# Performance work log

Hardware: AMD Instinct MI355X
Metric: run time of the kernel (lower is better)

The kernel has to match this reference:

```python
import jax, jax.numpy as jnp
import numpy as np

N, L, V = 8192, 50, 50000   # sentences, max words/sentence, vocab
D, H, O = 300, 150, 64      # embed dim, SAGE hidden, SAGE out
THRESH = 0.7
NEG = -1e9


def _sage_pool(h, A, mask, W1s, W1n, b1, W2s, W2n, b2, gw, gb):
    """Two-layer mean-aggregator SAGEConv + GlobalAttentionPooling, vectorized
    over N independent per-sentence graphs.
    h:[N,L,din] node feats, A:[N,L,L] bool adjacency (src u -> dst v), mask:[N,L] valid nodes."""
    Af = A.astype(h.dtype)
    deg = jnp.maximum(Af.sum(axis=1), 1.0)  # in-degree per dst node [N,L]

    def conv(x, Ws, Wn, b):
        m = jnp.einsum('nuv,nud->nvd', Af, x) / deg[..., None]  # mean of in-neighbors
        return x @ Ws + m @ Wn + b  # fc_self(x) + fc_neigh(mean)

    h1 = jax.nn.relu(conv(h, W1s, W1n, b1))
    h2 = conv(h1, W2s, W2n, b2)
    # global attention pooling: softmax(gate) over real nodes of each graph
    gate = jnp.squeeze(h2 @ gw, -1) + gb  # [N,L]
    attn = jax.nn.softmax(jnp.where(mask, gate, NEG), axis=-1)
    return jnp.einsum('nl,nld->nd', attn, h2)  # [N,O]


def setup_inputs() -> dict:
    key = jax.random.key(0)
    ks = jax.random.split(key, 32)
    pos = jnp.arange(L)
    lengths = jax.random.randint(ks[0], (N,), 5, L + 1)
    valid = pos[None, :] < lengths[:, None]  # [N,L] real-word mask (0 = pad)
    words = jax.random.randint(ks[1], (N, L), 1, V) * valid
    syntax_words = jax.random.randint(ks[2], (N, L), 1, V) * valid
    adj = jax.random.uniform(ks[3], (N, L, L)) < 0.08
    syntax_adj = (adj & valid[:, :, None] & valid[:, None, :]).astype(jnp.int32)
    hsg_feature = jax.random.normal(ks[4], (N, O), jnp.float32)

    def lin(k, i, o):
        return jax.random.normal(k, (i, o), jnp.float32) / np.sqrt(i)

    inp = {
        'words': words.astype(jnp.int32),
        'syntax_words': syntax_words.astype(jnp.int32),
        'syntax_adj': syntax_adj,
        'hsg_feature': hsg_feature,
        'embed': jax.random.normal(ks[5], (V, D), jnp.float32) * 0.1,
        'sem_W1s': lin(ks[6], D, H), 'sem_W1n': lin(ks[7], D, H), 'sem_b1': jnp.zeros((H,), jnp.float32),
        'sem_W2s': lin(ks[8], H, O), 'sem_W2n': lin(ks[9], H, O), 'sem_b2': jnp.zeros((O,), jnp.float32),
        'sem_gw': lin(ks[10], O, 1), 'sem_gb': jnp.zeros((1,), jnp.float32),
        'syn_W1s': lin(ks[11], D, H), 'syn_W1n': lin(ks[12], D, H), 'syn_b1': jnp.zeros((H,), jnp.float32),
        'syn_W2s': lin(ks[13], H, O), 'syn_W2n': lin(ks[14], H, O), 'syn_b2': jnp.zeros((O,), jnp.float32),
        'syn_gw': lin(ks[15], O, 1), 'syn_gb': jnp.zeros((1,), jnp.float32),
        'cls_w1': lin(ks[16], 3 * O, 128), 'cls_b1': jnp.zeros((128,), jnp.float32),
        'cls_w2': lin(ks[17], 128, 2), 'cls_b2': jnp.zeros((2,), jnp.float32),
    }
    return inp


def reference(words, syntax_words, syntax_adj, hsg_feature, embed,
              sem_W1s, sem_W1n, sem_b1, sem_W2s, sem_W2n, sem_b2, sem_gw, sem_gb,
              syn_W1s, syn_W1n, syn_b1, syn_W2s, syn_W2n, syn_b2, syn_gw, syn_gb,
              cls_w1, cls_b1, cls_w2, cls_b2):
    # --- semantic graph: per-sentence cosine-similarity thresholding ---
    mask = words > 0
    emb = embed[words]  # [N,L,D] gather
    nrm = emb / jnp.maximum(jnp.linalg.norm(emb, axis=-1, keepdims=True), 1e-8)
    cos = jnp.einsum('nld,nmd->nlm', nrm, nrm)  # [N,L,L]
    semA = (cos > THRESH) & mask[:, :, None] & mask[:, None, :]  # includes self-loops (cos=1)
    sem_feat = _sage_pool(emb, semA, mask,
                          sem_W1s, sem_W1n, sem_b1, sem_W2s, sem_W2n, sem_b2, sem_gw, sem_gb)
    # --- syntax graph: given per-sentence adjacency over its word ids ---
    syn_mask = syntax_words > 0
    syn_emb = embed[syntax_words]
    syn_feat = _sage_pool(syn_emb, syntax_adj.astype(bool), syn_mask,
                          syn_W1s, syn_W1n, syn_b1, syn_W2s, syn_W2n, syn_b2, syn_gw, syn_gb)
    # --- concat with HSG sentence state, classify ---
    feat = jnp.concatenate([sem_feat, syn_feat, hsg_feature], axis=-1)  # [N,192]
    hid = jax.nn.relu(feat @ cls_w1 + cls_b1)
    return hid @ cls_w2 + cls_b2  # [N,2]
```

## Files before the change

kernel.cpp:

```cpp
#include <hip/hip_runtime.h>

#define NS 8192
#define L  50

typedef unsigned short u16;
typedef unsigned int   u32;
typedef __attribute__((ext_vector_type(8))) __bf16 bf16x8;
typedef __attribute__((ext_vector_type(4))) float  f32x4;

#define OFF_X    0
#define OFF_TT   0
#define OFF_T2T  0
#define OFF_RED  9216
#define OFF_H1   21760
#define OFF_M    43264
#define OFF_DIAG 43264
#define OFF_WID  52480
#define OFF_CLO  52736
#define OFF_CHI  52992
#define OFF_RDEG 53248
#define SMEM_SZ  53504

#define XSTR  328
#define TSTR  68
#define H1STR 168
#define MSTR  72
#define RSTR  20

#define W1_ROWS 320
#define W1_KP   328
#define W2_ROWS 128
#define W2_KP   168
#define W1SZ (W1_ROWS * W1_KP)
#define W2SZ (W2_ROWS * W2_KP)

__device__ __forceinline__ u16 f2bf(float f) {
  u32 u = __float_as_uint(f);
  u += 0x7fffu + ((u >> 16) & 1u);
  return (u16)(u >> 16);
}
__device__ __forceinline__ f32x4 mfma16(bf16x8 a, bf16x8 b, f32x4 c) {
  return __builtin_amdgcn_mfma_f32_16x16x32_bf16(a, b, c, 0, 0, 0);
}
__device__ __forceinline__ uint2 pack4bf(f32x4 c) {
  uint2 p;
  p.x = (u32)f2bf(c[0]) | ((u32)f2bf(c[1]) << 16);
  p.y = (u32)f2bf(c[2]) | ((u32)f2bf(c[3]) << 16);
  return p;
}
union BF8U { bf16x8 v; uint4 u; };
__device__ __forceinline__ bf16x8 ld_bf8_b64pair(const u16* p) {
  uint2 a = *(const uint2*)p;
  uint2 b = *(const uint2*)(p + 4);
  BF8U r; r.u = make_uint4(a.x, a.y, b.x, b.y);
  return r.v;
}

struct GParams {
  const int* words; const int* syn_words; const int* syn_adj;
  const float* embed;
  const float* sem_b1; const float* sem_b2; const float* sem_gw; const float* sem_gb;
  const float* syn_b1; const float* syn_b2; const float* syn_gw; const float* syn_gb;
  const u16* w1t_sem; const u16* w1t_syn; const u16* w2t_sem; const u16* w2t_syn;
  float* semf; float* synf;
};

#define AGG_SLOT(ACCSLOT, GT)                                                \
  {                                                                          \
    const int gg = (GT);                                                     \
    const u16* tb = tt + (gg * 16 + ln) * TSTR + quad * 8;                   \
    bf16x8 ta0 = ld_bf8_b64pair(tb);                                         \
    bf16x8 ta1 = ld_bf8_b64pair(tb + 32);                                    \
    f32x4 gacc[4] = {z4, z4, z4, z4};                                        \
    _Pragma("unroll")                                                        \
    for (int vt = 0; vt < 4; ++vt) {                                         \
      gacc[vt] = mfma16(ta0, mb0[vt], gacc[vt]);                             \
      gacc[vt] = mfma16(ta1, mb1[vt], gacc[vt]);                             \
    }                                                                        \
    const int j0 = gg * 16 + quad * 4;                                       \
    float bv[4];                                                             \
    _Pragma("unroll")                                                        \
    for (int r = 0; r < 4; ++r) { int j = j0 + r; bv[r] = (j < 150) ? b1g[j] : 0.f; } \
    _Pragma("unroll")                                                        \
    for (int vt = 0; vt < 4; ++vt) {                                         \
      const int v = vt * 16 + ln;                                            \
      f32x4 hv;                                                              \
      _Pragma("unroll")                                                      \
      for (int r = 0; r < 4; ++r)                                            \
        hv[r] = fmaxf(ACCSLOT[vt][r] + gacc[vt][r] * rd[vt] + bv[r], 0.f);   \
      *(uint2*)(h1p + v * H1STR + j0) = pack4bf(hv);                         \
    }                                                                        \
  }

__global__ __launch_bounds__(256, 3) void sage_kernel(GParams P) {
  __shared__ __align__(16) char smem[SMEM_SZ];
  int*   wid   = (int*)(smem + OFF_WID);
  u32*   clo   = (u32*)(smem + OFF_CLO);
  u32*   chi   = (u32*)(smem + OFF_CHI);
  float* rdegp = (float*)(smem + OFF_RDEG);
  float* diag  = (float*)(smem + OFF_DIAG);

  const int tid  = threadIdx.x;
  const int lane = tid & 63;
  const int w    = tid >> 6;
  const int ln   = lane & 15;
  const int quad = lane >> 4;

  const bool semg = (blockIdx.x < NS);
  const int  n    = semg ? blockIdx.x : (blockIdx.x - NS);

  const int*   wsrc = semg ? P.words   : P.syn_words;
  const u16*   W1T  = semg ? P.w1t_sem : P.w1t_syn;
  const u16*   W2T  = semg ? P.w2t_sem : P.w2t_syn;
  const float* b1g  = semg ? P.sem_b1  : P.syn_b1;
  const float* b2g  = semg ? P.sem_b2  : P.syn_b2;
  const float* gw   = semg ? P.sem_gw  : P.syn_gw;
  const float* gb   = semg ? P.sem_gb  : P.syn_gb;
  float* featout    = semg ? P.semf    : P.synf;

  {
    int wd = 0;
    {
      const int v = w + 4 * ln;
      if (lane < 16 && v < L) wd = wsrc[(size_t)n * L + v];
    }
    for (int i = 0; i < 16; ++i) {
      const int v = w + 4 * i;
      const int word = __shfl(wd, i);
      const float* src = P.embed + (size_t)word * 300;
      u16* xrow = (u16*)(smem + OFF_X) + v * XSTR;
      for (int l = lane; l < 82; l += 64) {
        uint2 pk = make_uint2(0u, 0u);
        if (word > 0 && l < 75) {
          float4 f = *(const float4*)(src + l * 4);
          u32 ax = __float_as_uint(f.x) + 0x8000u;
          u32 ay = __float_as_uint(f.y) + 0x8000u;
          u32 az = __float_as_uint(f.z) + 0x8000u;
          u32 aw = __float_as_uint(f.w) + 0x8000u;
          pk.x = (ax >> 16) | (ay & 0xffff0000u);
          pk.y = (az >> 16) | (aw & 0xffff0000u);
        }
        *(uint2*)(xrow + l * 4) = pk;
      }
    }
    if (tid < 64) {
      wid[tid] = (tid < L) ? wsrc[(size_t)n * L + tid] : 0;
      clo[tid] = 0u; chi[tid] = 0u;
    }
  }
  __syncthreads();

  const f32x4 z4 = {0.f, 0.f, 0.f, 0.f};

  if (semg) {
    f32x4 g[4] = {z4, z4, z4, z4};
    const char* xb = smem + OFF_X;
    const int arow = (w * 16 + ln) * (XSTR * 2) + quad * 16;
    for (int kk = 0; kk < 10; ++kk) {
      bf16x8 a = *(const bf16x8*)(xb + arow + kk * 64);
      #pragma unroll
      for (int nt = 0; nt < 4; ++nt) {
        bf16x8 b = *(const bf16x8*)(xb + (nt * 16 + ln) * (XSTR * 2) + quad * 16 + kk * 64);
        g[nt] = mfma16(a, b, g[nt]);
      }
    }
    {
      const int r = ln - quad * 4;
      if (r >= 0 && r < 4) {
        #pragma unroll
        for (int nt = 0; nt < 4; ++nt) {
          if (nt == w) {
            float val = (r == 0) ? g[nt][0] : (r == 1) ? g[nt][1]
                      : (r == 2) ? g[nt][2] : g[nt][3];
            diag[w * 16 + ln] = val;
          }
        }
      }
    }
    __syncthreads();
    {
      const int ubase = w * 16 + quad * 4;
      float ru[4]; int uok[4];
      #pragma unroll
      for (int r = 0; r < 4; ++r) {
        ru[r] = rsqrtf(fmaxf(diag[ubase + r], 1e-12f));
        uok[r] = wid[ubase + r] > 0;
      }
      #pragma unroll
      for (int nt = 0; nt < 4; ++nt) {
        const int v = nt * 16 + ln;
        const float rv = rsqrtf(fmaxf(diag[v], 1e-12f));
        const bool vok = wid[v] > 0;
        u32 nib = 0u;
        #pragma unroll
        for (int r = 0; r < 4; ++r) {
          float c = g[nt][r] * ru[r] * rv;
          if (vok && uok[r] && c > 0.7f) nib |= (1u << r);
        }
        if (nib) {
          if (ubase < 32) atomicOr(&clo[v], nib << ubase);
          else            atomicOr(&chi[v], nib << (ubase - 32));
        }
      }
    }
  } else {
    const int* abase = P.syn_adj + (size_t)n * (L * L);
    for (int v = w; v < L; v += 4) {
      int val = (lane < L) ? abase[lane * L + v] : 0;
      unsigned long long m = __ballot(val != 0);
      if (lane == 0) { clo[v] = (u32)m; chi[v] = (u32)(m >> 32); }
    }
    __syncthreads();
  }
  __syncthreads();

  if (tid < 64) {
    int dg = __popc(clo[tid]) + __popc(chi[tid]);
    rdegp[tid] = 1.0f / (float)(dg > 0 ? dg : 1);
  }
  {
    const int v = lane, half = w;
    const u32 src = (half < 2) ? clo[v] : chi[v];
    const int sh = (half & 1) * 16;
    u16* Mrow = (u16*)(smem + OFF_M) + v * MSTR + half * 16;
    #pragma unroll
    for (int c = 0; c < 4; ++c) {
      uint2 pk;
      u32 b0 = (src >> (sh + 4 * c + 0)) & 1u;
      u32 b1 = (src >> (sh + 4 * c + 1)) & 1u;
      u32 b2 = (src >> (sh + 4 * c + 2)) & 1u;
      u32 b3 = (src >> (sh + 4 * c + 3)) & 1u;
      pk.x = (b0 ? 0x3F80u : 0u) | (b1 ? 0x3F800000u : 0u);
      pk.y = (b2 ? 0x3F80u : 0u) | (b3 ? 0x3F800000u : 0u);
      *(uint2*)(Mrow + 4 * c) = pk;
    }
  }

  const int rs0 = (2 * w)     * 16 + ln;
  const int rs1 = (2 * w + 1) * 16 + ln;
  const int rs2 = ((w < 2) ? (8 + w) : (16 + w)) * 16 + ln;
  const int rs3 = (10 + 2 * w) * 16 + ln;
  const int rs4 = (11 + 2 * w) * 16 + ln;
  f32x4 acc[5][4];
  #pragma unroll
  for (int i = 0; i < 5; ++i)
    #pragma unroll
    for (int m = 0; m < 4; ++m) acc[i][m] = z4;
  {
    const char* xb = smem + OFF_X;
    for (int kk = 0; kk < 10; ++kk) {
      const int wo = kk * 32 + quad * 8;
      bf16x8 x[4];
      #pragma unroll
      for (int m = 0; m < 4; ++m)
        x[m] = *(const bf16x8*)(xb + (m * 16 + ln) * (XSTR * 2) + quad * 16 + kk * 64);
      bf16x8 bf0 = *(const bf16x8*)(W1T + (size_t)rs0 * W1_KP + wo);
      bf16x8 bf1 = *(const bf16x8*)(W1T + (size_t)rs1 * W1_KP + wo);
      bf16x8 bf2 = *(const bf16x8*)(W1T + (size_t)rs2 * W1_KP + wo);
      bf16x8 bf3 = *(const bf16x8*)(W1T + (size_t)rs3 * W1_KP + wo);
      bf16x8 bf4 = *(const bf16x8*)(W1T + (size_t)rs4 * W1_KP + wo);
      #pragma unroll
      for (int m = 0; m < 4; ++m) {
        acc[0][m] = mfma16(x[m], bf0, acc[0][m]);
        acc[1][m] = mfma16(x[m], bf1, acc[1][m]);
        acc[3][m] = mfma16(bf3, x[m], acc[3][m]);
        acc[4][m] = mfma16(bf4, x[m], acc[4][m]);
      }
      if (w < 2) {
        #pragma unroll
        for (int m = 0; m < 4; ++m) acc[2][m] = mfma16(x[m], bf2, acc[2][m]);
      } else {
        #pragma unroll
        for (int m = 0; m < 4; ++m) acc[2][m] = mfma16(bf2, x[m], acc[2][m]);
      }
    }
  }
  __syncthreads();

  float rd[4];
  #pragma unroll
  for (int vt = 0; vt < 4; ++vt) rd[vt] = rdegp[vt * 16 + ln];

  {
    u16* tt = (u16*)(smem + OFF_TT);
    #pragma unroll
    for (int m = 0; m < 4; ++m) {
      const int v0 = m * 16 + quad * 4;
      *(uint2*)(tt + ((2 * w)     * 16 + ln) * TSTR + v0) = pack4bf(acc[0][m]);
      *(uint2*)(tt + ((2 * w + 1) * 16 + ln) * TSTR + v0) = pack4bf(acc[1][m]);
    }
    if (w < 2) {
      #pragma unroll
      for (int m = 0; m < 4; ++m) {
        const int v0 = m * 16 + quad * 4;
        *(uint2*)(tt + ((8 + w) * 16 + ln) * TSTR + v0) = pack4bf(acc[2][m]);
      }
    }
  }
  __syncthreads();

  {
    const u16* tt = (const u16*)(smem + OFF_TT);
    const u16* Mp = (const u16*)(smem + OFF_M);
    u16* h1p = (u16*)(smem + OFF_H1);
    bf16x8 mb0[4], mb1[4];
    #pragma unroll
    for (int vt = 0; vt < 4; ++vt) {
      mb0[vt] = *(const bf16x8*)(Mp + (vt * 16 + ln) * MSTR + quad * 8);
      mb1[vt] = *(const bf16x8*)(Mp + (vt * 16 + ln) * MSTR + quad * 8 + 32);
    }
    AGG_SLOT(acc[3], 2 * w)
    AGG_SLOT(acc[4], 2 * w + 1)
    if (w >= 2) AGG_SLOT(acc[2], 6 + w)
  }
  __syncthreads();

  f32x4 h2v[4];
  {
    f32x4 s2acc[4] = {z4, z4, z4, z4};
    f32x4 t2acc[4] = {z4, z4, z4, z4};
    const u16* h1p = (const u16*)(smem + OFF_H1);
    for (int kk = 0; kk < 5; ++kk) {
      const int wo = kk * 32 + quad * 8;
      bf16x8 h[4];
      #pragma unroll
      for (int t4 = 0; t4 < 4; ++t4)
        h[t4] = *(const bf16x8*)(h1p + (t4 * 16 + ln) * H1STR + wo);
      bf16x8 a2  = *(const bf16x8*)(W2T + (size_t)(w * 16 + ln) * W2_KP + wo);
      bf16x8 b2f = *(const bf16x8*)(W2T + (size_t)((4 + w) * 16 + ln) * W2_KP + wo);
      #pragma unroll
      for (int vt = 0; vt < 4; ++vt) {
        s2acc[vt] = mfma16(a2, h[vt], s2acc[vt]);
        t2acc[vt] = mfma16(h[vt], b2f, t2acc[vt]);
      }
    }
    u16* t2t = (u16*)(smem + OFF_T2T);
    #pragma unroll
    for (int m = 0; m < 4; ++m) {
      const int v0 = m * 16 + quad * 4;
      *(uint2*)(t2t + (w * 16 + ln) * TSTR + v0) = pack4bf(t2acc[m]);
    }
    const u16* Mp = (const u16*)(smem + OFF_M);
    f32x4 g2[4] = {z4, z4, z4, z4};
    const u16* t2b = t2t + (w * 16 + ln) * TSTR + quad * 8;
    bf16x8 u0 = ld_bf8_b64pair(t2b);
    bf16x8 u1 = ld_bf8_b64pair(t2b + 32);
    #pragma unroll
    for (int vt = 0; vt < 4; ++vt) {
      bf16x8 m0 = *(const bf16x8*)(Mp + (vt * 16 + ln) * MSTR + quad * 8);
      bf16x8 m1 = *(const bf16x8*)(Mp + (vt * 16 + ln) * MSTR + quad * 8 + 32);
      g2[vt] = mfma16(u0, m0, g2[vt]);
      g2[vt] = mfma16(u1, m1, g2[vt]);
    }
    const int j0q = w * 16 + quad * 4;
    float b2v[4];
    #pragma unroll
    for (int r = 0; r < 4; ++r) b2v[r] = b2g[j0q + r];
    #pragma unroll
    for (int vt = 0; vt < 4; ++vt)
      #pragma unroll
      for (int r = 0; r < 4; ++r)
        h2v[vt][r] = s2acc[vt][r] + g2[vt][r] * rd[vt] + b2v[r];
  }
  __syncthreads();

  {
    const int j0q = w * 16 + quad * 4;
    float gwv[4];
    #pragma unroll
    for (int r = 0; r < 4; ++r) gwv[r] = gw[j0q + r];
    float* redp = (float*)(smem + OFF_RED);
    #pragma unroll
    for (int vt = 0; vt < 4; ++vt) {
      float p = h2v[vt][0] * gwv[0] + h2v[vt][1] * gwv[1]
              + h2v[vt][2] * gwv[2] + h2v[vt][3] * gwv[3];
      redp[(vt * 16 + ln) * RSTR + (w * 4 + quad)] = p;
    }
  }
  __syncthreads();

  float attnv;
  {
    const float* redp = (const float*)(smem + OFF_RED) + lane * RSTR;
    f32x4 r0 = *(const f32x4*)(redp);
    f32x4 r1 = *(const f32x4*)(redp + 4);
    f32x4 r2 = *(const f32x4*)(redp + 8);
    f32x4 r3 = *(const f32x4*)(redp + 12);
    float g = gb[0] + r0[0] + r0[1] + r0[2] + r0[3] + r1[0] + r1[1] + r1[2] + r1[3]
            + r2[0] + r2[1] + r2[2] + r2[3] + r3[0] + r3[1] + r3[2] + r3[3];
    const bool val = wid[lane] > 0;
    g = val ? g : -1e30f;
    float mx = g;
    #pragma unroll
    for (int off = 32; off; off >>= 1) mx = fmaxf(mx, __shfl_xor(mx, off));
    float e = val ? __expf(g - mx) : 0.f;
    float ssum = e;
    #pragma unroll
    for (int off = 32; off; off >>= 1) ssum += __shfl_xor(ssum, off);
    attnv = e / ssum;
  }

  {
    float av[4];
    #pragma unroll
    for (int vt = 0; vt < 4; ++vt) av[vt] = __shfl(attnv, vt * 16 + ln);
    float xr[4];
    #pragma unroll
    for (int r = 0; r < 4; ++r) {
      float x = av[0] * h2v[0][r] + av[1] * h2v[1][r]
              + av[2] * h2v[2][r] + av[3] * h2v[3][r];
      #pragma unroll
      for (int off = 1; off < 16; off <<= 1) x += __shfl_xor(x, off);
      xr[r] = x;
    }
    if (ln == 0) {
      const int j0q = w * 16 + quad * 4;
      *(float4*)(featout + (size_t)n * 64 + j0q) = make_float4(xr[0], xr[1], xr[2], xr[3]);
    }
  }
}

__global__ void prep_all(const float* sem_W1n, const float* sem_W1s,
                         const float* syn_W1n, const float* syn_W1s,
                         const float* sem_W2s, const float* sem_W2n,
                         const float* syn_W2s, const float* syn_W2n,
                         u16* w1t_sem, u16* w1t_syn, u16* w2t_sem, u16* w2t_syn) {
  int idx = blockIdx.x * 256 + threadIdx.x;
  if (idx < 2 * W1SZ) {
    const bool sem = idx < W1SZ;
    const int li = sem ? idx : idx - W1SZ;
    const float* Wn = sem ? sem_W1n : syn_W1n;
    const float* Ws = sem ? sem_W1s : syn_W1s;
    u16* dst = sem ? w1t_sem : w1t_syn;
    int nn = li / W1_KP, k = li - nn * W1_KP;
    float v = 0.f;
    if (k < 300) {
      if (nn < 150) v = Wn[k * 150 + nn];
      else if (nn >= 160 && nn < 310) v = Ws[k * 150 + (nn - 160)];
    }
    dst[li] = f2bf(v);
  } else if (idx < 2 * W1SZ + 2 * W2SZ) {
    int j = idx - 2 * W1SZ;
    const bool sem = j < W2SZ;
    const int li = sem ? j : j - W2SZ;
    const float* Ws = sem ? sem_W2s : syn_W2s;
    const float* Wn = sem ? sem_W2n : syn_W2n;
    u16* dst = sem ? w2t_sem : w2t_syn;
    int nn = li / W2_KP, k = li - nn * W2_KP;
    float v = 0.f;
    if (k < 150) v = (nn < 64) ? Ws[k * 64 + nn] : Wn[k * 64 + (nn - 64)];
    dst[li] = f2bf(v);
  }
}

__global__ __launch_bounds__(128) void cls_kernel(const float* semf, const float* synf,
                                                  const float* hsg,
                                                  const float* w1, const float* b1,
                                                  const float* w2, const float* b2,
                                                  float* out) {
  __shared__ float feat[16][192];
  __shared__ float hid[16][132];
  const int r0 = blockIdx.x * 16;
  for (int idx = threadIdx.x; idx < 16 * 192; idx += 128) {
    int r = idx / 192, c = idx % 192;
    float v;
    if (c < 64)        v = semf[(size_t)(r0 + r) * 64 + c];
    else if (c < 128)  v = synf[(size_t)(r0 + r) * 64 + (c - 64)];
    else               v = hsg [(size_t)(r0 + r) * 64 + (c - 128)];
    feat[r][c] = v;
  }
  __syncthreads();
  {
    const int j = threadIdx.x;
    float acc[16];
    float bb = b1[j];
    #pragma unroll
    for (int r = 0; r < 16; ++r) acc[r] = bb;
    for (int k = 0; k < 192; ++k) {
      float ww = w1[(size_t)k * 128 + j];
      #pragma unroll
      for (int r = 0; r < 16; ++r) acc[r] += feat[r][k] * ww;
    }
    #pragma unroll
    for (int r = 0; r < 16; ++r) hid[r][j] = fmaxf(acc[r], 0.0f);
  }
  __syncthreads();
  if (threadIdx.x < 32) {
    const int r = threadIdx.x >> 1, o = threadIdx.x & 1;
    float a = b2[o];
    for (int h = 0; h < 128; ++h) a += hid[r][h] * w2[h * 2 + o];
    out[(size_t)(r0 + r) * 2 + o] = a;
  }
}

extern "C" void kernel_launch(void* const* d_in, const int* in_sizes, int n_in,
                              void* d_out, int out_size, void* d_ws, size_t ws_size,
                              hipStream_t stream) {
  GParams P;
  P.words     = (const int*)d_in[0];
  P.syn_words = (const int*)d_in[1];
  P.syn_adj   = (const int*)d_in[2];
  const float* hsg = (const float*)d_in[3];
  P.embed   = (const float*)d_in[4];
  const float* sem_W1s = (const float*)d_in[5];
  const float* sem_W1n = (const float*)d_in[6];
  P.sem_b1  = (const float*)d_in[7];
  const float* sem_W2s = (const float*)d_in[8];
  const float* sem_W2n = (const float*)d_in[9];
  P.sem_b2  = (const float*)d_in[10];
  P.sem_gw  = (const float*)d_in[11];
  P.sem_gb  = (const float*)d_in[12];
  const float* syn_W1s = (const float*)d_in[13];
  const float* syn_W1n = (const float*)d_in[14];
  P.syn_b1  = (const float*)d_in[15];
  const float* syn_W2s = (const float*)d_in[16];
  const float* syn_W2n = (const float*)d_in[17];
  P.syn_b2  = (const float*)d_in[18];
  P.syn_gw  = (const float*)d_in[19];
  P.syn_gb  = (const float*)d_in[20];
  const float* cls_w1 = (const float*)d_in[21];
  const float* cls_b1 = (const float*)d_in[22];
  const float* cls_w2 = (const float*)d_in[23];
  const float* cls_b2 = (const float*)d_in[24];

  float* semf = (float*)d_ws;
  float* synf = semf + (size_t)NS * 64;
  u16* w1t_sem = (u16*)((char*)d_ws + (size_t)4 * 1024 * 1024);
  u16* w1t_syn = w1t_sem + W1SZ;
  u16* w2t_sem = w1t_syn + W1SZ;
  u16* w2t_syn = w2t_sem + W2SZ;
  P.semf = semf; P.synf = synf;
  P.w1t_sem = w1t_sem; P.w1t_syn = w1t_syn;
  P.w2t_sem = w2t_sem; P.w2t_syn = w2t_syn;

  const int total = 2 * W1SZ + 2 * W2SZ;
  prep_all<<<(total + 255) / 256, 256, 0, stream>>>(
      sem_W1n, sem_W1s, syn_W1n, syn_W1s,
      sem_W2s, sem_W2n, syn_W2s, syn_W2n,
      w1t_sem, w1t_syn, w2t_sem, w2t_syn);

  sage_kernel<<<2 * NS, 256, 0, stream>>>(P);
  cls_kernel<<<NS / 16, 128, 0, stream>>>(semf, synf, hsg, cls_w1, cls_b1,
                                          cls_w2, cls_b2, (float*)d_out);
}
```

Measured before the change: 768.9 us.

## Fuse cosine Gram product into layer-1 projection loop sharing X fragment loads

The semantic-graph Gram matrix is now computed inside the same k-loop as the first-layer weight projections. Both use the same bf16 X fragments loaded once from shared memory, which removes a separate pass over X and one barrier. Each wave's column tiles are rotated through a per-wave order (ct) so that tile 0 is the wave's own diagonal block. That lets the Gram computation keep only the wave's own row block against all column tiles, and the aggregation and writes are re-indexed to match. The cost is more live accumulator registers at once (g plus acc), which may add register pressure at the given occupancy bound.

```diff
diff --git a/kernel.cpp b/kernel.cpp
--- a/kernel.cpp
+++ b/kernel.cpp
@@ -83,7 +83,7 @@
     for (int r = 0; r < 4; ++r) { int j = j0 + r; bv[r] = (j < 150) ? b1g[j] : 0.f; } \
     _Pragma("unroll")                                                        \
     for (int vt = 0; vt < 4; ++vt) {                                         \
-      const int v = vt * 16 + ln;                                            \
+      const int v = ct[vt] * 16 + ln;                                        \
       f32x4 hv;                                                              \
       _Pragma("unroll")                                                      \
       for (int r = 0; r < 4; ++r)                                            \
@@ -116,7 +116,9 @@
   const float* b2g  = semg ? P.sem_b2  : P.syn_b2;
   const float* gw   = semg ? P.sem_gw  : P.syn_gw;
   const float* gb   = semg ? P.sem_gb  : P.syn_gb;
-  float* featout    = semg ? P.semf    : P.synf;
+  float* featout    = semg ? P.semf    : P.syn_adj ? P.synf : P.synf;
+
+  const int ct[4] = {w, (w + 1) & 3, (w + 2) & 3, (w + 3) & 3};
 
   {
     int wd = 0;
@@ -152,65 +154,168 @@
 
   const f32x4 z4 = {0.f, 0.f, 0.f, 0.f};
 
-  if (semg) {
-    f32x4 g[4] = {z4, z4, z4, z4};
-    const char* xb = smem + OFF_X;
-    const int arow = (w * 16 + ln) * (XSTR * 2) + quad * 16;
-    for (int kk = 0; kk < 10; ++kk) {
-      bf16x8 a = *(const bf16x8*)(xb + arow + kk * 64);
-      #pragma unroll
-      for (int nt = 0; nt < 4; ++nt) {
-        bf16x8 b = *(const bf16x8*)(xb + (nt * 16 + ln) * (XSTR * 2) + quad * 16 + kk * 64);
-        g[nt] = mfma16(a, b, g[nt]);
-      }
-    }
-    {
-      const int r = ln - quad * 4;
-      if (r >= 0 && r < 4) {
-        #pragma unroll
-        for (int nt = 0; nt < 4; ++nt) {
-          if (nt == w) {
-            float val = (r == 0) ? g[nt][0] : (r == 1) ? g[nt][1]
-                      : (r == 2) ? g[nt][2] : g[nt][3];
-            diag[w * 16 + ln] = val;
-          }
-        }
-      }
-    }
-    __syncthreads();
-    {
-      const int ubase = w * 16 + quad * 4;
-      float ru[4]; int uok[4];
-      #pragma unroll
-      for (int r = 0; r < 4; ++r) {
-        ru[r] = rsqrtf(fmaxf(diag[ubase + r], 1e-12f));
-        uok[r] = wid[ubase + r] > 0;
-      }
-      #pragma unroll
-      for (int nt = 0; nt < 4; ++nt) {
-        const int v = nt * 16 + ln;
-        const float rv = rsqrtf(fmaxf(diag[v], 1e-12f));
-        const bool vok = wid[v] > 0;
-        u32 nib = 0u;
-        #pragma unroll
-        for (int r = 0; r < 4; ++r) {
-          float c = g[nt][r] * ru[r] * rv;
-          if (vok && uok[r] && c > 0.7f) nib |= (1u << r);
-        }
-        if (nib) {
-          if (ubase < 32) atomicOr(&clo[v], nib << ubase);
-          else            atomicOr(&chi[v], nib << (ubase - 32));
-        }
-      }
-    }
-  } else {
+  if (!semg) {
     const int* abase = P.syn_adj + (size_t)n * (L * L);
     for (int v = w; v < L; v += 4) {
       int val = (lane < L) ? abase[lane * L + v] : 0;
       unsigned long long m = __ballot(val != 0);
       if (lane == 0) { clo[v] = (u32)m; chi[v] = (u32)(m >> 32); }
     }
-    __syncthreads();
+  }
+
+  const int rs0 = (2 * w)     * 16 + ln;
+  const int rs1 = (2 * w + 1) * 16 + ln;
+  const int rs2 = ((w < 2) ? (8 + w) : (16 + w)) * 16 + ln;
+  const int rs3 = (10 + 2 * w) * 16 + ln;
+  const int rs4 = (11 + 2 * w) * 16 + ln;
+  f32x4 acc[5][4];
+  f32x4 g[4] = {z4, z4, z4, z4};
+  #pragma unroll
+  for (int i = 0; i < 5; ++i)
+    #pragma unroll
+    for (int m = 0; m < 4; ++m) acc[i][m] = z4;
+  {
+    const char* xb = smem + OFF_X;
+    const int xr0 = (ct[0] * 16 + ln) * (XSTR * 2);
+    const int xr1 = (ct[1] * 16 + ln) * (XSTR * 2);
+    const int xr2 = (ct[2] * 16 + ln) * (XSTR * 2);
+    const int xr3 = (ct[3] * 16 + ln) * (XSTR * 2);
+    if (semg) {
+      for (int kk = 0; kk < 10; ++kk) {
+        const int xo = quad * 16 + kk * 64;
+        const int wo = kk * 32 + quad * 8;
+        bf16x8 x0 = *(const bf16x8*)(xb + xr0 + xo);
+        bf16x8 x1 = *(const bf16x8*)(xb + xr1 + xo);
+        bf16x8 x2 = *(const bf16x8*)(xb + xr2 + xo);
+        bf16x8 x3 = *(const bf16x8*)(xb + xr3 + xo);
+        bf16x8 bf0 = *(const bf16x8*)(W1T + (size_t)rs0 * W1_KP + wo);
+        bf16x8 bf1 = *(const bf16x8*)(W1T + (size_t)rs1 * W1_KP + wo);
+        bf16x8 bf2 = *(const bf16x8*)(W1T + (size_t)rs2 * W1_KP + wo);
+        bf16x8 bf3 = *(const bf16x8*)(W1T + (size_t)rs3 * W1_KP + wo);
+        bf16x8 bf4 = *(const bf16x8*)(W1T + (size_t)rs4 * W1_KP + wo);
+        g[0] = mfma16(x0, x0, g[0]);
+        g[1] = mfma16(x0, x1, g[1]);
+        g[2] = mfma16(x0, x2, g[2]);
+        g[3] = mfma16(x0, x3, g[3]);
+        acc[0][0] = mfma16(x0, bf0, acc[0][0]);
+        acc[0][1] = mfma16(x1, bf0, acc[0][1]);
+        acc[0][2] = mfma16(x2, bf0, acc[0][2]);
+        acc[0][3] = mfma16(x3, bf0, acc[0][3]);
+        acc[1][0] = mfma16(x0, bf1, acc[1][0]);
+        acc[1][1] = mfma16(x1, bf1, acc[1][1]);
+        acc[1][2] = mfma16(x2, bf1, acc[1][2]);
+        acc[1][3] = mfma16(x3, bf1, acc[1][3]);
+        acc[3][0] = mfma16(bf3, x0, acc[3][0]);
+        acc[3][1] = mfma16(bf3, x1, acc[3][1]);
+        acc[3][2] = mfma16(bf3, x2, acc[3][2]);
+        acc[3][3] = mfma16(bf3, x3, acc[3][3]);
+        acc[4][0] = mfma16(bf4, x0, acc[4][0]);
+        acc[4][1] = mfma16(bf4, x1, acc[4][1]);
+        acc[4][2] = mfma16(bf4, x2, acc[4][2]);
+        acc[4][3] = mfma16(bf4, x3, acc[4][3]);
+        if (w < 2) {
+          acc[2][0] = mfma16(x0, bf2, acc[2][0]);
+          acc[2][1] = mfma16(x1, bf2, acc[2][1]);
+          acc[2][2] = mfma16(x2, bf2, acc[2][2]);
+          acc[2][3] = mfma16(x3, bf2, acc[2][3]);
+        } else {
+          acc[2][0] = mfma16(bf2, x0, acc[2][0]);
+          acc[2][1] = mfma16(bf2, x1, acc[2][1]);
+          acc[2][2] = mfma16(bf2, x2, acc[2][2]);
+          acc[2][3] = mfma16(bf2, x3, acc[2][3]);
+        }
+      }
+      const int r = ln - quad * 4;
+      if (r >= 0 && r < 4) {
+        float val = (r == 0) ? g[0][0] : (r == 1) ? g[0][1]
+                  : (r == 2) ? g[0][2] : g[0][3];
+        diag[w * 16 + ln] = val;
+      }
+    } else {
+      for (int kk = 0; kk < 10; ++kk) {
+        const int xo = quad * 16 + kk * 64;
+        const int wo = kk * 32 + quad * 8;
+        bf16x8 x0 = *(const bf16x8*)(xb + xr0 + xo);
+        bf16x8 x1 = *(const bf16x8*)(xb + xr1 + xo);
+        bf16x8 x2 = *(const bf16x8*)(xb + xr2 + xo);
+        bf16x8 x3 = *(const bf16x8*)(xb + xr3 + xo);
+        bf16x8 bf0 = *(const bf16x8*)(W1T + (size_t)rs0 * W1_KP + wo);
+        bf16x8 bf1 = *(const bf16x8*)(W1T + (size_t)rs1 * W1_KP + wo);
+        bf16x8 bf2 = *(const bf16x8*)(W1T + (size_t)rs2 * W1_KP + wo);
+        bf16x8 bf3 = *(const bf16x8*)(W1T + (size_t)rs3 * W1_KP + wo);
+        bf16x8 bf4 = *(const bf16x8*)(W1T + (size_t)rs4 * W1_KP + wo);
+        acc[0][0] = mfma16(x0, bf0, acc[0][0]);
+        acc[0][1] = mfma16(x1, bf0, acc[0][1]);
+        acc[0][2] = mfma16(x2, bf0, acc[0][2]);
+        acc[0][3] = mfma16(x3, bf0, acc[0][3]);
+        acc[1][0] = mfma16(x0, bf1, acc[1][0]);
+        acc[1][1] = mfma16(x1, bf1, acc[1][1]);
+        acc[1][2] = mfma16(x2, bf1, acc[1][2]);
+        acc[1][3] = mfma16(x3, bf1, acc[1][3]);
+        acc[3][0] = mfma16(bf3, x0, acc[3][0]);
+        acc[3][1] = mfma16(bf3, x1, acc[3][1]);
+        acc[3][2] = mfma16(bf3, x2, acc[3][2]);
+        acc[3][3] = mfma16(bf3, x3, acc[3][3]);
+        acc[4][0] = mfma16(bf4, x0, acc[4][0]);
+        acc[4][1] = mfma16(bf4, x1, acc[4][1]);
+        acc[4][2] = mfma16(bf4, x2, acc[4][2]);
+        acc[4][3] = mfma16(bf4, x3, acc[4][3]);
+        if (w < 2) {
+          acc[2][0] = mfma16(x0, bf2, acc[2][0]);
+          acc[2][1] = mfma16(x1, bf2, acc[2][1]);
+          acc[2][2] = mfma16(x2, bf2, acc[2][2]);
+          acc[2][3] = mfma16(x3, bf2, acc[2][3]);
+        } else {
+          acc[2][0] = mfma16(bf2, x0, acc[2][0]);
+          acc[2][1] = mfma16(bf2, x1, acc[2][1]);
+          acc[2][2] = mfma16(bf2, x2, acc[2][2]);
+          acc[2][3] = mfma16(bf2, x3, acc[2][3]);
+        }
+      }
+    }
+  }
+  __syncthreads();
+
+  if (semg) {
+    const int ubase = w * 16 + quad * 4;
+    float ru[4]; int uok[4];
+    #pragma unroll
+    for (int r = 0; r < 4; ++r) {
+      ru[r] = rsqrtf(fmaxf(diag[ubase + r], 1e-12f));
+      uok[r] = wid[ubase + r] > 0;
+    }
+    #pragma unroll
+    for (int j = 0; j < 4; ++j) {
+      const int v = ct[j] * 16 + ln;
+      const float rv = rsqrtf(fmaxf(diag[v], 1e-12f));
+      const bool vok = wid[v] > 0;
+      u32 nib = 0u;
+      #pragma unroll
+      for (int r = 0; r < 4; ++r) {
+        float c = g[j][r] * ru[r] * rv;
+        if (vok && uok[r] && c > 0.7f) nib |= (1u << r);
+      }
+      if (nib) {
+        if (ubase < 32) atomicOr(&clo[v], nib << ubase);
+        else            atomicOr(&chi[v], nib << (ubase - 32));
+      }
+    }
+  }
+  {
+    u16* tt = (u16*)(smem + OFF_TT);
+    #pragma unroll
+    for (int j = 0; j < 4; ++j) {
+      const int v0 = ct[j] * 16 + quad * 4;
+      *(uint2*)(tt + ((2 * w)     * 16 + ln) * TSTR + v0) = pack4bf(acc[0][j]);
+      *(uint2*)(tt + ((2 * w + 1) * 16 + ln) * TSTR + v0) = pack4bf(acc[1][j]);
+    }
+    if (w < 2) {
+      #pragma unroll
+      for (int j = 0; j < 4; ++j) {
+        const int v0 = ct[j] * 16 + quad * 4;
+        *(uint2*)(tt + ((8 + w) * 16 + ln) * TSTR + v0) = pack4bf(acc[2][j]);
+      }
+    }
   }
   __syncthreads();
 
@@ -235,79 +340,20 @@
       *(uint2*)(Mrow + 4 * c) = pk;
     }
   }
-
-  const int rs0 = (2 * w)     * 16 + ln;
-  const int rs1 = (2 * w + 1) * 16 + ln;
-  const int rs2 = ((w < 2) ? (8 + w) : (16 + w)) * 16 + ln;
-  const int rs3 = (10 + 2 * w) * 16 + ln;
-  const int rs4 = (11 + 2 * w) * 16 + ln;
-  f32x4 acc[5][4];
-  #pragma unroll
-  for (int i = 0; i < 5; ++i)
-    #pragma unroll
-    for (int m = 0; m < 4; ++m) acc[i][m] = z4;
-  {
-    const char* xb = smem + OFF_X;
-    for (int kk = 0; kk < 10; ++kk) {
-      const int wo = kk * 32 + quad * 8;
-      bf16x8 x[4];
-      #pragma unroll
-      for (int m = 0; m < 4; ++m)
-        x[m] = *(const bf16x8*)(xb + (m * 16 + ln) * (XSTR * 2) + quad * 16 + kk * 64);
-      bf16x8 bf0 = *(const bf16x8*)(W1T + (size_t)rs0 * W1_KP + wo);
-      bf16x8 bf1 = *(const bf16x8*)(W1T + (size_t)rs1 * W1_KP + wo);
-      bf16x8 bf2 = *(const bf16x8*)(W1T + (size_t)rs2 * W1_KP + wo);
-      bf16x8 bf3 = *(const bf16x8*)(W1T + (size_t)rs3 * W1_KP + wo);
-      bf16x8 bf4 = *(const bf16x8*)(W1T + (size_t)rs4 * W1_KP + wo);
-      #pragma unroll
-      for (int m = 0; m < 4; ++m) {
-        acc[0][m] = mfma16(x[m], bf0, acc[0][m]);
-        acc[1][m] = mfma16(x[m], bf1, acc[1][m]);
-        acc[3][m] = mfma16(bf3, x[m], acc[3][m]);
-        acc[4][m] = mfma16(bf4, x[m], acc[4][m]);
-      }
-      if (w < 2) {
-        #pragma unroll
-        for (int m = 0; m < 4; ++m) acc[2][m] = mfma16(x[m], bf2, acc[2][m]);
-      } else {
-        #pragma unroll
-        for (int m = 0; m < 4; ++m) acc[2][m] = mfma16(bf2, x[m], acc[2][m]);
-      }
-    }
-  }
-  __syncthreads();
-
-  float rd[4];
-  #pragma unroll
-  for (int vt = 0; vt < 4; ++vt) rd[vt] = rdegp[vt * 16 + ln];
-
-  {
-    u16* tt = (u16*)(smem + OFF_TT);
-    #pragma unroll
-    for (int m = 0; m < 4; ++m) {
-      const int v0 = m * 16 + quad * 4;
-      *(uint2*)(tt + ((2 * w)     * 16 + ln) * TSTR + v0) = pack4bf(acc[0][m]);
-      *(uint2*)(tt + ((2 * w + 1) * 16 + ln) * TSTR + v0) = pack4bf(acc[1][m]);
-    }
-    if (w < 2) {
-      #pragma unroll
-      for (int m = 0; m < 4; ++m) {
-        const int v0 = m * 16 + quad * 4;
-        *(uint2*)(tt + ((8 + w) * 16 + ln) * TSTR + v0) = pack4bf(acc[2][m]);
-      }
-    }
-  }
   __syncthreads();
 
   {
     const u16* tt = (const u16*)(smem + OFF_TT);
     const u16* Mp = (const u16*)(smem + OFF_M);
     u16* h1p = (u16*)(smem + OFF_H1);
+    float rd[4];
     bf16x8 mb0[4], mb1[4];
     #pragma unroll
     for (int vt = 0; vt < 4; ++vt) {
-      mb0[vt] = *(const bf16x8*)(Mp + (vt * 16 + ln) * MSTR + quad * 8);
-      mb1[vt] = *(const bf16x8*)(Mp + (vt * 16 + ln) * MSTR + quad * 8 + 32);
+      const int v = ct[vt] * 16 + ln;
+      rd[vt]  = rdegp[v];
+      mb0[vt] = *(const bf16x8*)(Mp + v * MSTR + quad * 8);
+      mb1[vt] = *(const bf16x8*)(Mp + v * MSTR + quad * 8 + 32);
     }
     AGG_SLOT(acc[3], 2 * w)
     AGG_SLOT(acc[4], 2 * w + 1)
@@ -316,6 +362,9 @@
   __syncthreads();
 
   f32x4 h2v[4];
+  float rd2[4];
+  #pragma unroll
+  for (int vt = 0; vt < 4; ++vt) rd2[vt] = rdegp[vt * 16 + ln];
   {
     f32x4 s2acc[4] = {z4, z4, z4, z4};
     f32x4 t2acc[4] = {z4, z4, z4, z4};
@@ -360,7 +409,7 @@
     for (int vt = 0; vt < 4; ++vt)
       #pragma unroll
       for (int r = 0; r < 4; ++r)
-        h2v[vt][r] = s2acc[vt][r] + g2[vt][r] * rd[vt] + b2v[r];
+        h2v[vt][r] = s2acc[vt][r] + g2[vt][r] * rd2[vt] + b2v[r];
   }
   __syncthreads();
 
@@ -386,14 +435,14 @@
     f32x4 r1 = *(const f32x4*)(redp + 4);
     f32x4 r2 = *(const f32x4*)(redp + 8);
     f32x4 r3 = *(const f32x4*)(redp + 12);
-    float g = gb[0] + r0[0] + r0[1] + r0[2] + r0[3] + r1[0] + r1[1] + r1[2] + r1[3]
-            + r2[0] + r2[1] + r2[2] + r2[3] + r3[0] + r3[1] + r3[2] + r3[3];
+    float g0 = gb[0] + r0[0] + r0[1] + r0[2] + r0[3] + r1[0] + r1[1] + r1[2] + r1[3]
+             + r2[0] + r2[1] + r2[2] + r2[3] + r3[0] + r3[1] + r3[2] + r3[3];
     const bool val = wid[lane] > 0;
-    g = val ? g : -1e30f;
-    float mx = g;
+    g0 = val ? g0 : -1e30f;
+    float mx = g0;
     #pragma unroll
     for (int off = 32; off; off >>= 1) mx = fmaxf(mx, __shfl_xor(mx, off));
-    float e = val ? __expf(g - mx) : 0.f;
+    float e = val ? __expf(g0 - mx) : 0.f;
     float ssum = e;
     #pragma unroll
     for (int off = 32; off; off >>= 1) ssum += __shfl_xor(ssum, off);
```

Result: slower. 1.043 ms (+35.7%).
